# Optimization experiments

Measured on AMD Instinct MI355X. Metric: run time of the kernel, lower is better.

The kernel has to match this reference:

```python
import jax, jax.numpy as jnp
import numpy as np

B = 524288      # batch
F = 32          # nr_features
C = 10          # nr_classes
H = 64          # hidden_size
D = 2           # tree_depth
NN = 2 ** D - 1 # internal nodes
NL = 2 ** D     # leaf nodes
EPS = 1e-5

# Static tree routing tables, reproducing the original Python int() (truncate-toward-zero) math exactly.
NODE_IDX = np.array([[int((2 ** (d - 1) * (2 ** D + l) - 2 ** D) / 2 ** D) for d in range(D)] for l in range(NL)])  # [NL, D]
PSIGN = np.array([[int(l / 2 ** (D - d)) % 2 for d in range(D)] for l in range(NL)])  # [NL, D]


def _linear_params(key, out_f, in_f):
    k1, k2 = jax.random.split(key)
    bound = 1.0 / np.sqrt(in_f)
    w = jax.random.uniform(k1, (out_f, in_f), minval=-bound, maxval=bound, dtype=jnp.float32)
    b = jax.random.uniform(k2, (out_f,), minval=-bound, maxval=bound, dtype=jnp.float32)
    return w, b


def setup_inputs() -> dict:
    key = jax.random.key(0)
    ks = jax.random.split(key, 6)
    x = jax.random.normal(ks[0], (B, F), dtype=jnp.float32)
    w_in, b_in = _linear_params(ks[1], H, F)
    bn_g = jnp.ones((H,), dtype=jnp.float32)   # BatchNorm1d weight init to 1
    bn_b = jnp.zeros((H,), dtype=jnp.float32)  # BatchNorm1d bias init to 0
    w_fi, b_fi = _linear_params(ks[2], NN * F, H)
    w_fs, b_fs = _linear_params(ks[3], NN * F, H)
    w_lc, b_lc = _linear_params(ks[4], NL * C, H)
    return {"x": x, "w_in": w_in, "b_in": b_in, "bn_g": bn_g, "bn_b": bn_b,
            "w_fi": w_fi, "b_fi": b_fi, "w_fs": w_fs, "b_fs": b_fs,
            "w_lc": w_lc, "b_lc": b_lc}


def reference(x, w_in, b_in, bn_g, bn_b, w_fi, b_fi, w_fs, b_fs, w_lc, b_lc):
    inp = x  # raw features used inside the tree gating
    # input layer + BatchNorm1d (training-mode batch stats, biased var) + exact GELU
    h = x @ w_in.T + b_in                                   # [B, H]
    mu = jnp.mean(h, axis=0)
    var = jnp.var(h, axis=0)
    h = (h - mu) / jnp.sqrt(var + EPS) * bn_g + bn_b
    h = jax.nn.gelu(h, approximate=False)

    fi = (h @ w_fi.T + b_fi).reshape(B, NN, F)              # feature importances per node
    fs = (h @ w_fs.T + b_fs).reshape(B, NN, F)              # feature splits per node
    lc = (h @ w_lc.T + b_lc).reshape(B, NL, C)              # leaf class logits

    smx = jax.nn.softmax(fi, axis=-1)                        # [B, NN, F]
    # node_sd = sigmoid(sum(smx*input) - sum(smx*fs))
    sd = jax.nn.sigmoid(jnp.einsum('bnf,bnf->bn', smx, inp[:, None, :] - fs))  # [B, NN]

    # gate per (leaf, depth): sd if p==0 else 1-sd, at the statically-computed node index
    g = sd[:, NODE_IDX]                                      # [B, NL, D]
    g = jnp.where(PSIGN[None, :, :] == 0, g, 1.0 - g)
    coeff = jnp.prod(g, axis=-1)                             # [B, NL]

    out = jnp.einsum('blc,bl->bc', lc, coeff)                # [B, C]
    return out
```

## Files before the change

kernel.cpp:

```cpp
#include <hip/hip_runtime.h>

typedef __attribute__((ext_vector_type(8))) __bf16 bf16x8;
typedef __attribute__((ext_vector_type(4))) float f32x4;
typedef unsigned short u16;
typedef unsigned int u32;

#define NB 524288
#define EPSI 1e-5f
#define NSHADOW 16

__device__ __forceinline__ float bf2f(u16 h) {
    union { u32 u; float f; } cv; cv.u = ((u32)h) << 16; return cv.f;
}
__device__ __forceinline__ u16 f2bf(float f) {
    __bf16 b = (__bf16)f; return __builtin_bit_cast(u16, b);
}
__device__ __forceinline__ float ldany(const void* p, long i, int isf) {
    return isf ? ((const float*)p)[i] : bf2f(((const u16*)p)[i]);
}

__device__ __forceinline__ float fast_gelu(float v) {
    float t = 1.5957691216057308f * v * (1.0f + 0.044715f * v * v);
    float en = __expf(-t);
    return v * __builtin_amdgcn_rcpf(1.0f + en);
}

template<typename T>
__device__ __forceinline__ void load8f(const T* p, float* o);
template<>
__device__ __forceinline__ void load8f<__bf16>(const __bf16* p, float* o) {
    bf16x8 r = *reinterpret_cast<const bf16x8*>(p);
#pragma unroll
    for (int i = 0; i < 8; ++i) o[i] = (float)r[i];
}
template<>
__device__ __forceinline__ void load8f<float>(const float* p, float* o) {
    f32x4 a = *reinterpret_cast<const f32x4*>(p);
    f32x4 b = *reinterpret_cast<const f32x4*>(p + 4);
#pragma unroll
    for (int i = 0; i < 4; ++i) { o[i] = a[i]; o[4 + i] = b[i]; }
}

__device__ __forceinline__ bf16x8 loadfrag(const __bf16* p) {
    return *reinterpret_cast<const bf16x8*>(p);
}
__device__ __forceinline__ bf16x8 loadfrag(const float* p) {
    f32x4 a = *reinterpret_cast<const f32x4*>(p);
    f32x4 b = *reinterpret_cast<const f32x4*>(p + 4);
    bf16x8 r;
#pragma unroll
    for (int i = 0; i < 4; ++i) { r[i] = (__bf16)a[i]; r[4 + i] = (__bf16)b[i]; }
    return r;
}

__device__ __forceinline__ int detect_isf(const void* x) {
    const int lane = threadIdx.x & 63;
    u32 w0 = ((const u32*)x)[lane];
    u32 w1 = ((const u32*)x)[64 + lane];
    int hit = ((((w0 >> 7) & 0xFFu) >= 0xC0u) || (((w1 >> 7) & 0xFFu) >= 0xC0u)) ? 1 : 0;
    return __ballot(hit) != 0ull;
}

template<int CTRL>
__device__ __forceinline__ float dpp_rot_add(float v) {
    int s = __builtin_amdgcn_update_dpp(0, __builtin_bit_cast(int, v), CTRL, 0xF, 0xF, false);
    return v + __builtin_bit_cast(float, s);
}
__device__ __forceinline__ float row_reduce_add(float v) {
    v = dpp_rot_add<0x121>(v);
    v = dpp_rot_add<0x122>(v);
    v = dpp_rot_add<0x124>(v);
    v = dpp_rot_add<0x128>(v);
    return v;
}

template<typename T>
__device__ __forceinline__ void stats_body(const T* __restrict__ x,
                                           const T* __restrict__ w_in,
                                           float* __restrict__ ws,
                                           float* __restrict__ red) {
    const int lane = threadIdx.x & 63;
    const int wave = threadIdx.x >> 6;
    const int c = lane & 15;
    const int q = lane >> 4;

    bf16x8 b1[4];
#pragma unroll
    for (int nt = 0; nt < 4; ++nt)
        b1[nt] = loadfrag(w_in + (nt * 16 + c) * 32 + q * 8);

    float accs[4][4], accq[4][4];
#pragma unroll
    for (int nt = 0; nt < 4; ++nt)
#pragma unroll
        for (int r = 0; r < 4; ++r) { accs[nt][r] = 0.f; accq[nt][r] = 0.f; }

    const int wid = blockIdx.x * 4 + wave;
    for (int t = 0; t < 4; ++t) {
        const long row0 = ((long)wid * 4 + t) * 16;
        bf16x8 a1 = loadfrag(x + (row0 + c) * 32 + q * 8);
#pragma unroll
        for (int nt = 0; nt < 4; ++nt) {
            f32x4 z = {0.f, 0.f, 0.f, 0.f};
            f32x4 acc = __builtin_amdgcn_mfma_f32_16x16x32_bf16(a1, b1[nt], z, 0, 0, 0);
#pragma unroll
            for (int r = 0; r < 4; ++r) {
                float v = acc[r];
                accs[nt][r] += v;
                accq[nt][r] += v * v;
            }
        }
    }
    for (int i = threadIdx.x; i < 128; i += 256) red[i] = 0.f;
    __syncthreads();
#pragma unroll
    for (int nt = 0; nt < 4; ++nt) {
        float s  = accs[nt][0] + accs[nt][1] + accs[nt][2] + accs[nt][3];
        float sq = accq[nt][0] + accq[nt][1] + accq[nt][2] + accq[nt][3];
        s  += __shfl_xor(s, 16);  s  += __shfl_xor(s, 32);
        sq += __shfl_xor(sq, 16); sq += __shfl_xor(sq, 32);
        if (q == 0) {
            atomicAdd(&red[nt * 16 + c], s);
            atomicAdd(&red[64 + nt * 16 + c], sq);
        }
    }
    __syncthreads();
    float* shard = ws + (blockIdx.x & (NSHADOW - 1)) * 128;
    for (int i = threadIdx.x; i < 128; i += 256) atomicAdd(&shard[i], red[i]);
}

__global__ __launch_bounds__(256) void stats_kernel(
    const void* x, const void* w_in, const void* w_fi, const void* b_fi,
    const void* w_fs, const void* b_fs, const void* w_lc, const void* b_lc,
    float* __restrict__ ws)
{
    const int isf = detect_isf(x);

    if (blockIdx.x < 24) {
        u16* W2p = (u16*)(ws + 2176);
        const int idx = blockIdx.x * 256 + threadIdx.x;
        const int g = idx >> 6, f = idx & 63;
        float v = 0.f;
        if (g < 32)                 v = ldany(w_fi, (long)g * 64 + f, isf);
        else if (g < 64)            v = ldany(w_fs, (long)(g - 32) * 64 + f, isf);
        else if (g < 74)            v = ldany(w_lc, (long)(g - 64) * 64 + f, isf)
                                      + ldany(w_lc, (long)(g - 54) * 64 + f, isf);
        else if (g >= 80 && g < 90) v = ldany(w_lc, (long)(g - 60) * 64 + f, isf)
                                      + ldany(w_lc, (long)(g - 50) * 64 + f, isf);
        W2p[idx] = f2bf(v);
    } else if (blockIdx.x == 24 && threadIdx.x < 96) {
        float* biasP = ws + 2048;
        const int g = threadIdx.x;
        float v = 0.f;
        if (g < 32)                 v = ldany(b_fi, g, isf);
        else if (g < 64)            v = ldany(b_fs, g - 32, isf);
        else if (g < 74)            v = ldany(b_lc, g - 64, isf) + ldany(b_lc, g - 54, isf);
        else if (g >= 80 && g < 90) v = ldany(b_lc, g - 60, isf) + ldany(b_lc, g - 50, isf);
        biasP[g] = v;
    }

    __shared__ float red[128];
    if (isf) stats_body<float>((const float*)x, (const float*)w_in, ws, red);
    else     stats_body<__bf16>((const __bf16*)x, (const __bf16*)w_in, ws, red);
}

template<typename T>
__device__ __forceinline__ void main_body(
    const T* __restrict__ x, const T* __restrict__ bn_g, const T* __restrict__ bn_b,
    const T* __restrict__ w_in, const float* __restrict__ ws,
    const float* __restrict__ sums, T* __restrict__ out)
{
    const int lane = threadIdx.x & 63;
    const int wave = threadIdx.x >> 6;
    const int c = lane & 15;
    const int q = lane >> 4;
    const float* biasP = ws + 2048;
    const u16* W2p = (const u16*)(ws + 2176);

    bf16x8 b1[4];
#pragma unroll
    for (int nt = 0; nt < 4; ++nt) {
        const int row = 32 * (nt >> 1) + 8 * (c >> 2) + 4 * (nt & 1) + (c & 3);
        float mu  = sums[row] * (1.0f / NB);
        float var = fmaxf(sums[64 + row] * (1.0f / NB) - mu * mu, 0.0f);
        float s   = (float)bn_g[row] * rsqrtf(var + EPSI);
        float w8[8];
        load8f(w_in + row * 32 + q * 8, w8);
        bf16x8 f;
#pragma unroll
        for (int j = 0; j < 8; ++j) f[j] = (__bf16)(w8[j] * s);
        b1[nt] = f;
    }

    float shift_t[4][4];
#pragma unroll
    for (int nt = 0; nt < 4; ++nt)
#pragma unroll
        for (int r = 0; r < 4; ++r) {
            const int ft = 32 * (nt >> 1) + 8 * q + 4 * (nt & 1) + r;
            float mu  = sums[ft] * (1.0f / NB);
            float var = fmaxf(sums[64 + ft] * (1.0f / NB) - mu * mu, 0.0f);
            float s   = (float)bn_g[ft] * rsqrtf(var + EPSI);
            shift_t[nt][r] = (float)bn_b[ft] - mu * s;
        }

    bf16x8 b2[6][2];
#pragma unroll
    for (int nt = 0; nt < 6; ++nt)
#pragma unroll
        for (int kt = 0; kt < 2; ++kt)
            b2[nt][kt] = *reinterpret_cast<const bf16x8*>(W2p + (nt * 16 + c) * 64 + kt * 32 + q * 8);

    const float bfi0 = biasP[c],      bfi1 = biasP[16 + c];
    const float bfs0 = biasP[32 + c], bfs1 = biasP[48 + c];
    const float bu   = biasP[64 + c], bv   = biasP[80 + c];

    const long gw = (long)blockIdx.x * 4 + wave;
#pragma unroll 2
    for (int t = 0; t < 4; ++t) {
        const long row0 = gw * 64 + (long)t * 16;
        bf16x8 a1 = loadfrag(x + (row0 + c) * 32 + q * 8);

        float xv0[4], xv1[4];
#pragma unroll
        for (int r = 0; r < 4; ++r) {
            xv0[r] = (float)x[(row0 + q * 4 + r) * 32 + c];
            xv1[r] = (float)x[(row0 + q * 4 + r) * 32 + 16 + c];
        }

        f32x4 h4[4];
#pragma unroll
        for (int nt = 0; nt < 4; ++nt) {
            f32x4 z = {0.f, 0.f, 0.f, 0.f};
            h4[nt] = __builtin_amdgcn_mfma_f32_16x16x32_bf16(b1[nt], a1, z, 0, 0, 0);
        }

        bf16x8 a2_0, a2_1;
#pragma unroll
        for (int nt = 0; nt < 2; ++nt)
#pragma unroll
            for (int r = 0; r < 4; ++r) {
                a2_0[nt * 4 + r] = (__bf16)fast_gelu(h4[nt][r] + shift_t[nt][r]);
                a2_1[nt * 4 + r] = (__bf16)fast_gelu(h4[2 + nt][r] + shift_t[2 + nt][r]);
            }

        f32x4 acc[6];
#pragma unroll
        for (int nt = 0; nt < 6; ++nt) {
            f32x4 z = {0.f, 0.f, 0.f, 0.f};
            acc[nt] = __builtin_amdgcn_mfma_f32_16x16x32_bf16(a2_0, b2[nt][0], z, 0, 0, 0);
            acc[nt] = __builtin_amdgcn_mfma_f32_16x16x32_bf16(a2_1, b2[nt][1], acc[nt], 0, 0, 0);
        }

#pragma unroll
        for (int r = 0; r < 4; ++r) {
            float e0  = __expf(acc[0][r] + bfi0);
            float e1  = __expf(acc[1][r] + bfi1);
            float fs0 = acc[2][r] + bfs0;
            float fs1 = acc[3][r] + bfs1;
            float es = row_reduce_add(e0 + e1);
            float dp = row_reduce_add(e0 * (xv0[r] - fs0) + e1 * (xv1[r] - fs1));
            float d  = dp * __builtin_amdgcn_rcpf(es);
            float sd = __builtin_amdgcn_rcpf(1.0f + __expf(-d));
            float uu = acc[4][r] + bu, vv = acc[5][r] + bv;
            float o = sd * (vv + sd * (uu - vv));
            if (c < 10) out[(row0 + q * 4 + r) * 10 + c] = (T)o;
        }
    }
}

__global__ __launch_bounds__(256, 4) void main_kernel(
    const void* x, const void* bn_g, const void* bn_b, const void* w_in,
    float* ws, void* outv)
{
    __shared__ float sums[128];
    if (threadIdx.x < 128) {
        float s = 0.f;
#pragma unroll
        for (int k = 0; k < NSHADOW; ++k) s += ws[k * 128 + threadIdx.x];
        sums[threadIdx.x] = s;
    }
    __syncthreads();

    if (detect_isf(x))
        main_body<float>((const float*)x, (const float*)bn_g, (const float*)bn_b,
                         (const float*)w_in, ws, sums, (float*)outv);
    else
        main_body<__bf16>((const __bf16*)x, (const __bf16*)bn_g, (const __bf16*)bn_b,
                          (const __bf16*)w_in, ws, sums, (__bf16*)outv);
}

extern "C" void kernel_launch(void* const* d_in, const int* in_sizes, int n_in,
                              void* d_out, int out_size, void* d_ws, size_t ws_size,
                              hipStream_t stream) {
    float* ws = (float*)d_ws;
    hipMemsetAsync(d_ws, 0, NSHADOW * 128 * sizeof(float), stream);
    stats_kernel<<<2048, 256, 0, stream>>>(d_in[0], d_in[1], d_in[5], d_in[6],
                                           d_in[7], d_in[8], d_in[9], d_in[10], ws);
    main_kernel<<<2048, 256, 0, stream>>>(d_in[0], d_in[3], d_in[4], d_in[1], ws, d_out);
}
```

Before: 169.6 us.

## Stage MFMA weight fragments in LDS and double grid size

Per-block weight fragments (BN-scaled W_in, W2) and BN shift values are now built cooperatively once per block into shared memory and reloaded from LDS inside the row loop, instead of every lane holding them in registers. An opaque asm zero offset stops the compiler from hoisting those LDS loads back into registers. Each wave now processes 32 rows instead of 64 and the grid is doubled to 4096 blocks. The aim is to cut VGPR pressure and raise occupancy, at the cost of extra LDS reads per tile and more per-block setup work.

```diff
diff --git a/kernel.cpp b/kernel.cpp
--- a/kernel.cpp
+++ b/kernel.cpp
@@ -167,49 +167,57 @@
 template<typename T>
 __device__ __forceinline__ void main_body(
     const T* __restrict__ x, const T* __restrict__ bn_g, const T* __restrict__ bn_b,
-    const T* __restrict__ w_in, const float* __restrict__ ws,
-    const float* __restrict__ sums, T* __restrict__ out)
+    const T* __restrict__ w_in, const float* __restrict__ ws, T* __restrict__ out,
+    float* __restrict__ sums, float* __restrict__ shs,
+    u16* __restrict__ w1s, u16* __restrict__ w2s)
 {
-    const int lane = threadIdx.x & 63;
-    const int wave = threadIdx.x >> 6;
+    const int tid = threadIdx.x;
+    const int lane = tid & 63;
+    const int wave = tid >> 6;
     const int c = lane & 15;
     const int q = lane >> 4;
     const float* biasP = ws + 2048;
-    const u16* W2p = (const u16*)(ws + 2176);
-
-    bf16x8 b1[4];
-#pragma unroll
-    for (int nt = 0; nt < 4; ++nt) {
-        const int row = 32 * (nt >> 1) + 8 * (c >> 2) + 4 * (nt & 1) + (c & 3);
+
+    if (tid < 128) {
+        float s = 0.f;
+#pragma unroll
+        for (int k = 0; k < NSHADOW; ++k) s += ws[k * 128 + tid];
+        sums[tid] = s;
+    }
+    __syncthreads();
+
+    {
+        const int nt = tid >> 6, l = tid & 63, cc = l & 15, qq = l >> 4;
+        const int row = 32 * (nt >> 1) + 8 * (cc >> 2) + 4 * (nt & 1) + (cc & 3);
         float mu  = sums[row] * (1.0f / NB);
         float var = fmaxf(sums[64 + row] * (1.0f / NB) - mu * mu, 0.0f);
         float s   = (float)bn_g[row] * rsqrtf(var + EPSI);
         float w8[8];
-        load8f(w_in + row * 32 + q * 8, w8);
+        load8f(w_in + row * 32 + qq * 8, w8);
         bf16x8 f;
 #pragma unroll
         for (int j = 0; j < 8; ++j) f[j] = (__bf16)(w8[j] * s);
-        b1[nt] = f;
-    }
-
-    float shift_t[4][4];
-#pragma unroll
-    for (int nt = 0; nt < 4; ++nt)
-#pragma unroll
-        for (int r = 0; r < 4; ++r) {
-            const int ft = 32 * (nt >> 1) + 8 * q + 4 * (nt & 1) + r;
-            float mu  = sums[ft] * (1.0f / NB);
-            float var = fmaxf(sums[64 + ft] * (1.0f / NB) - mu * mu, 0.0f);
-            float s   = (float)bn_g[ft] * rsqrtf(var + EPSI);
-            shift_t[nt][r] = (float)bn_b[ft] - mu * s;
-        }
-
-    bf16x8 b2[6][2];
-#pragma unroll
-    for (int nt = 0; nt < 6; ++nt)
-#pragma unroll
-        for (int kt = 0; kt < 2; ++kt)
-            b2[nt][kt] = *reinterpret_cast<const bf16x8*>(W2p + (nt * 16 + c) * 64 + kt * 32 + q * 8);
+        *reinterpret_cast<bf16x8*>(w1s + tid * 8) = f;
+    }
+    if (tid < 64) {
+        const int qq = tid >> 4, nt = (tid >> 2) & 3, r = tid & 3;
+        const int ft = 32 * (nt >> 1) + 8 * qq + 4 * (nt & 1) + r;
+        float mu  = sums[ft] * (1.0f / NB);
+        float var = fmaxf(sums[64 + ft] * (1.0f / NB) - mu * mu, 0.0f);
+        float s   = (float)bn_g[ft] * rsqrtf(var + EPSI);
+        shs[tid] = (float)bn_b[ft] - mu * s;
+    }
+    {
+        const u32* W2p32 = (const u32*)(ws + 2176);
+        for (int k = tid; k < 768; k += 256) {
+            const int f = k >> 6, l = k & 63, cc = l & 15, qq = l >> 4;
+            const int nt = f >> 1, kt = f & 1;
+            const u32* src = W2p32 + ((nt * 16 + cc) * 64 + kt * 32 + qq * 8) / 2;
+            u32* dst = (u32*)(w2s + k * 8);
+            dst[0] = src[0]; dst[1] = src[1]; dst[2] = src[2]; dst[3] = src[3];
+        }
+    }
+    __syncthreads();
 
     const float bfi0 = biasP[c],      bfi1 = biasP[16 + c];
     const float bfs0 = biasP[32 + c], bfs1 = biasP[48 + c];
@@ -217,8 +225,14 @@
 
     const long gw = (long)blockIdx.x * 4 + wave;
 #pragma unroll 2
-    for (int t = 0; t < 4; ++t) {
-        const long row0 = gw * 64 + (long)t * 16;
+    for (int t = 0; t < 2; ++t) {
+        u32 tweak = 0;
+        asm volatile("" : "+v"(tweak));
+        const u16* w1b = w1s + tweak;
+        const u16* w2b = w2s + tweak;
+        const float* shb = shs + tweak;
+
+        const long row0 = gw * 32 + (long)t * 16;
         bf16x8 a1 = loadfrag(x + (row0 + c) * 32 + q * 8);
 
         float xv0[4], xv1[4];
@@ -231,25 +245,31 @@
         f32x4 h4[4];
 #pragma unroll
         for (int nt = 0; nt < 4; ++nt) {
+            bf16x8 b1f = *reinterpret_cast<const bf16x8*>(w1b + (nt * 64 + lane) * 8);
             f32x4 z = {0.f, 0.f, 0.f, 0.f};
-            h4[nt] = __builtin_amdgcn_mfma_f32_16x16x32_bf16(b1[nt], a1, z, 0, 0, 0);
+            h4[nt] = __builtin_amdgcn_mfma_f32_16x16x32_bf16(b1f, a1, z, 0, 0, 0);
         }
 
         bf16x8 a2_0, a2_1;
 #pragma unroll
-        for (int nt = 0; nt < 2; ++nt)
+        for (int nt = 0; nt < 2; ++nt) {
+            f32x4 shA = *reinterpret_cast<const f32x4*>(shb + q * 16 + nt * 4);
+            f32x4 shB = *reinterpret_cast<const f32x4*>(shb + q * 16 + (2 + nt) * 4);
 #pragma unroll
             for (int r = 0; r < 4; ++r) {
-                a2_0[nt * 4 + r] = (__bf16)fast_gelu(h4[nt][r] + shift_t[nt][r]);
-                a2_1[nt * 4 + r] = (__bf16)fast_gelu(h4[2 + nt][r] + shift_t[2 + nt][r]);
+                a2_0[nt * 4 + r] = (__bf16)fast_gelu(h4[nt][r] + shA[r]);
+                a2_1[nt * 4 + r] = (__bf16)fast_gelu(h4[2 + nt][r] + shB[r]);
             }
+        }
 
         f32x4 acc[6];
 #pragma unroll
         for (int nt = 0; nt < 6; ++nt) {
+            bf16x8 f0 = *reinterpret_cast<const bf16x8*>(w2b + ((nt * 2 + 0) * 64 + lane) * 8);
+            bf16x8 f1 = *reinterpret_cast<const bf16x8*>(w2b + ((nt * 2 + 1) * 64 + lane) * 8);
             f32x4 z = {0.f, 0.f, 0.f, 0.f};
-            acc[nt] = __builtin_amdgcn_mfma_f32_16x16x32_bf16(a2_0, b2[nt][0], z, 0, 0, 0);
-            acc[nt] = __builtin_amdgcn_mfma_f32_16x16x32_bf16(a2_1, b2[nt][1], acc[nt], 0, 0, 0);
+            acc[nt] = __builtin_amdgcn_mfma_f32_16x16x32_bf16(a2_0, f0, z, 0, 0, 0);
+            acc[nt] = __builtin_amdgcn_mfma_f32_16x16x32_bf16(a2_1, f1, acc[nt], 0, 0, 0);
         }
 
 #pragma unroll
@@ -274,20 +294,16 @@
     float* ws, void* outv)
 {
     __shared__ float sums[128];
-    if (threadIdx.x < 128) {
-        float s = 0.f;
-#pragma unroll
-        for (int k = 0; k < NSHADOW; ++k) s += ws[k * 128 + threadIdx.x];
-        sums[threadIdx.x] = s;
-    }
-    __syncthreads();
+    __shared__ float shs[64];
+    __shared__ __attribute__((aligned(16))) u16 w1s[4 * 64 * 8];
+    __shared__ __attribute__((aligned(16))) u16 w2s[12 * 64 * 8];
 
     if (detect_isf(x))
         main_body<float>((const float*)x, (const float*)bn_g, (const float*)bn_b,
-                         (const float*)w_in, ws, sums, (float*)outv);
+                         (const float*)w_in, ws, (float*)outv, sums, shs, w1s, w2s);
     else
         main_body<__bf16>((const __bf16*)x, (const __bf16*)bn_g, (const __bf16*)bn_b,
-                          (const __bf16*)w_in, ws, sums, (__bf16*)outv);
+                          (const __bf16*)w_in, ws, (__bf16*)outv, sums, shs, w1s, w2s);
 }
 
 extern "C" void kernel_launch(void* const* d_in, const int* in_sizes, int n_in,
@@ -297,5 +313,5 @@
     hipMemsetAsync(d_ws, 0, NSHADOW * 128 * sizeof(float), stream);
     stats_kernel<<<2048, 256, 0, stream>>>(d_in[0], d_in[1], d_in[5], d_in[6],
                                            d_in[7], d_in[8], d_in[9], d_in[10], ws);
-    main_kernel<<<2048, 256, 0, stream>>>(d_in[0], d_in[3], d_in[4], d_in[1], ws, d_out);
-}
+    main_kernel<<<4096, 256, 0, stream>>>(d_in[0], d_in[3], d_in[4], d_in[1], ws, d_out);
+}
```

Result: faster. 155.6 us (-8.2%).
